# Optimization experiments

Hardware: AMD Instinct MI355X
Metric: run time of the kernel (lower is better)

## Reference

```python
import jax, jax.numpy as jnp
import numpy as np

B, N, C, H, WS, RANK = 64, 197, 768, 12, 14, 24
HD = C // H
SCALE = HD ** -0.5
NUM_REL = (2 * WS - 1) * (2 * WS - 1) + 3  # 732


def _make_rel_pos_index():
    coords = np.stack(np.meshgrid(np.arange(WS), np.arange(WS), indexing='ij'))  # [2,14,14]
    cf = coords.reshape(2, -1)  # [2,196]
    rel = (cf[:, :, None] - cf[:, None, :]).transpose(1, 2, 0)  # [196,196,2]
    rel = rel.copy()
    rel[..., 0] += WS - 1
    rel[..., 1] += WS - 1
    rel[..., 0] *= 2 * WS - 1
    idx = np.zeros((N, N), dtype=np.int32)
    idx[1:, 1:] = rel.sum(-1)
    idx[0, :] = NUM_REL - 3
    idx[:, 0] = NUM_REL - 2
    idx[0, 0] = NUM_REL - 1
    return idx


def setup_inputs() -> dict:
    key = jax.random.key(0)
    ks = jax.random.split(key, 13)
    s = lambda k, shape, sc=0.02: jax.random.normal(k, shape, jnp.float32) * sc
    return {
        'x': jax.random.normal(ks[0], (B, N, C), jnp.float32),
        'qkv_w': s(ks[1], (3 * C, C)),
        'q_bias': s(ks[2], (C,)),
        'v_bias': s(ks[3], (C,)),
        'q_lora_a': s(ks[4], (RANK, C)),
        'q_lora_b': s(ks[5], (C, RANK)),
        'k_lora_a': s(ks[6], (RANK, C)),
        'k_lora_b': s(ks[7], (C, RANK)),
        'v_lora_a': s(ks[8], (RANK, C)),
        'v_lora_b': s(ks[9], (C, RANK)),
        'rel_pos_table': s(ks[10], (NUM_REL, H)),
        'proj_w': s(ks[11], (C, C)),
        'proj_b': s(ks[12], (C,)),
        'rel_pos_index': jnp.asarray(_make_rel_pos_index()),
    }


def reference(x, qkv_w, q_bias, v_bias, q_lora_a, q_lora_b, k_lora_a, k_lora_b,
              v_lora_a, v_lora_b, rel_pos_table, proj_w, proj_b, rel_pos_index):
    lora = lambda a, b: jnp.einsum('bnc,rc,dr->bnd', x, a, b)  # rank-RANK adapter, scalar 1.0
    qkv_bias = jnp.concatenate([q_bias, jnp.zeros_like(v_bias), v_bias])
    qkv = x @ qkv_w.T + qkv_bias  # [B,N,3C]
    qkv = qkv + jnp.concatenate([lora(q_lora_a, q_lora_b),
                                 lora(k_lora_a, k_lora_b),
                                 lora(v_lora_a, v_lora_b)], axis=-1)
    qkv = qkv.reshape(B, N, 3, H, HD).transpose(2, 0, 3, 1, 4)  # [3,B,H,N,HD]
    q, k, v = qkv[0] * SCALE, qkv[1], qkv[2]
    attn = jnp.einsum('bhnd,bhmd->bhnm', q.astype(jnp.float32), k.astype(jnp.float32))
    rpb = rel_pos_table[rel_pos_index.reshape(-1)].reshape(N, N, H).transpose(2, 0, 1)
    attn = attn + rpb[None].astype(attn.dtype)
    attn = jax.nn.softmax(attn, axis=-1).astype(x.dtype)
    out = jnp.einsum('bhnm,bhmd->bhnd', attn, v).transpose(0, 2, 1, 3).reshape(B, N, C)
    return out @ proj_w.T + proj_b
```

## Files before the change

### kernel.cpp

```cpp
#include <hip/hip_runtime.h>

typedef __bf16 bf16;
typedef __attribute__((ext_vector_type(8))) __bf16 bf16x8;
typedef __attribute__((ext_vector_type(4))) __bf16 bf16x4;
typedef __attribute__((ext_vector_type(4))) float f32x4;

#define B_    64
#define N_    197
#define C_    768
#define H_    12
#define HD_   64
#define SCALE_ 0.125f
#define NM_   (N_*N_)
#define M_    (B_*N_)
#define NEGI_ (-30000.0f)
#define VTP_  200

#define GLL16(gptr, lptr) \
  __builtin_amdgcn_global_load_lds((const __attribute__((address_space(1))) unsigned int*)(gptr), \
                                   (__attribute__((address_space(3))) unsigned int*)(lptr), 16, 0, 0)

__global__ __launch_bounds__(256) void prep_kernel(
    const float* __restrict__ x, const float* __restrict__ pw,
    const float* __restrict__ qkv_w, const float* __restrict__ q_bias, const float* __restrict__ v_bias,
    const float* __restrict__ qa, const float* __restrict__ qb,
    const float* __restrict__ ka, const float* __restrict__ kb,
    const float* __restrict__ va, const float* __restrict__ vb,
    const float* __restrict__ table, const int* __restrict__ rpi,
    bf16* __restrict__ xbf, bf16* __restrict__ pwbf,
    bf16* __restrict__ weff, float* __restrict__ biasf, bf16* __restrict__ rpbT)
{
  const int bid = blockIdx.x, tid = threadIdx.x;
  if (bid < 5016) {
    const size_t n1 = (size_t)M_ * C_;
    size_t i8 = ((size_t)bid * 256 + tid) * 8;
    const float* src; bf16* dst; size_t off;
    if (i8 < n1) { src = x;  dst = xbf;  off = i8; }
    else         { src = pw; dst = pwbf; off = i8 - n1; }
    float4 f0 = *(const float4*)(src + off);
    float4 f1 = *(const float4*)(src + off + 4);
    bf16x8 v8;
    v8[0] = (bf16)f0.x; v8[1] = (bf16)f0.y; v8[2] = (bf16)f0.z; v8[3] = (bf16)f0.w;
    v8[4] = (bf16)f1.x; v8[5] = (bf16)f1.y; v8[6] = (bf16)f1.z; v8[7] = (bf16)f1.w;
    *(bf16x8*)(dst + off) = v8;
  } else if (bid < 11928) {
    int idx = (bid - 5016) * 256 + tid;
    int d = idx / C_, c = idx - d * C_;
    int sel = d / C_, dd = d - sel * C_;
    const float* a  = (sel == 0) ? qa : (sel == 1) ? ka : va;
    const float* bw = (sel == 0) ? qb : (sel == 1) ? kb : vb;
    float acc = qkv_w[idx];
#pragma unroll
    for (int r = 0; r < 24; ++r)
      acc += bw[dd * 24 + r] * a[r * C_ + c];
    weff[idx] = (bf16)acc;
    if (c == 0)
      biasf[d] = (sel == 0) ? q_bias[dd] : (sel == 2) ? v_bias[dd] : 0.0f;
  } else {
    int idx = (bid - 11928) * 256 + tid;
    if (idx < H_ * NM_) {
      int h = idx / NM_, nm = idx - h * NM_;
      int n = nm / N_, m = nm - n * N_;
      rpbT[((size_t)h * N_ + m) * VTP_ + n] = (bf16)table[rpi[nm] * H_ + h];
    }
  }
}

template<int MODE>
__global__ __launch_bounds__(256, 4) void gemm_bt(
    const bf16* __restrict__ A, const bf16* __restrict__ Bw,
    const float* __restrict__ biasp,
    float* __restrict__ Coutf, int M, int Nn, int K,
    bf16* __restrict__ qo, bf16* __restrict__ ko, bf16* __restrict__ vo)
{
  __shared__ __align__(16) bf16 As[128 * 64];
  __shared__ __align__(16) bf16 Bs[128 * 64];
  const int tid = threadIdx.x;
  const int lane = tid & 63, w = tid >> 6;
  const int l15 = lane & 15, quad = lane >> 4;
  const int wm = (w & 1) * 64, wn = (w >> 1) * 64;
  const int rowA0 = blockIdx.y * 128;
  const int rowB0 = blockIdx.x * 128;

  f32x4 acc[4][4] = {};

  for (int kt = 0; kt < K; kt += 64) {
#pragma unroll
    for (int i = 0; i < 4; ++i) {
      int lin = (w * 4 + i) * 64 + lane;
      int r  = lin >> 3;
      int cb = lin & 7;
      int csw = ((cb ^ (r & 7)) << 3);
      int ga = rowA0 + r; if (ga > M - 1) ga = M - 1;
      GLL16(A + (size_t)ga * K + kt + csw, &As[lin * 8]);
      int gb = rowB0 + r; if (gb > Nn - 1) gb = Nn - 1;
      GLL16(Bw + (size_t)gb * K + kt + csw, &Bs[lin * 8]);
    }
    __syncthreads();
#pragma unroll
    for (int ks = 0; ks < 2; ++ks) {
      const int cb = ks * 4 + quad;
      const int sw = (cb ^ (l15 & 7)) << 3;
      bf16x8 af[4], bfr[4];
#pragma unroll
      for (int i = 0; i < 4; ++i)
        af[i] = *(const bf16x8*)(&As[(wm + i * 16 + l15) * 64 + sw]);
#pragma unroll
      for (int j = 0; j < 4; ++j)
        bfr[j] = *(const bf16x8*)(&Bs[(wn + j * 16 + l15) * 64 + sw]);
#pragma unroll
      for (int i = 0; i < 4; ++i)
#pragma unroll
        for (int j = 0; j < 4; ++j)
          acc[i][j] = __builtin_amdgcn_mfma_f32_16x16x32_bf16(af[i], bfr[j], acc[i][j], 0, 0, 0);
    }
    __syncthreads();
  }

#pragma unroll
  for (int i = 0; i < 4; ++i) {
#pragma unroll
    for (int j = 0; j < 4; ++j) {
#pragma unroll
      for (int r = 0; r < 4; ++r) {
        int m = rowA0 + wm + i * 16 + quad * 4 + r;
        int d = rowB0 + wn + j * 16 + l15;
        if (m >= M) continue;
        float v = acc[i][j][r] + biasp[d];
        if (MODE == 0) {
          int b = m / N_, n = m - b * N_;
          int sel = d / C_, dd = d - sel * C_;
          int h = dd >> 6, hd = dd & 63;
          if (sel == 0)
            qo[(((size_t)b * H_ + h) * N_ + n) * HD_ + hd] = (bf16)(v * SCALE_);
          else if (sel == 1)
            ko[(((size_t)b * H_ + h) * N_ + n) * HD_ + hd] = (bf16)v;
          else
            vo[(((size_t)b * H_ + h) * HD_ + hd) * VTP_ + n] = (bf16)v;
        } else {
          Coutf[(size_t)m * Nn + d] = v;
        }
      }
    }
  }
}

#define SW 232
__global__ __launch_bounds__(256) void attn_kernel(
    const bf16* __restrict__ q, const bf16* __restrict__ k, const bf16* __restrict__ vT_g,
    const bf16* __restrict__ rpbT, bf16* __restrict__ out)
{
  __shared__ __align__(16) bf16 s_lds[64 * SW];

  const int tid = threadIdx.x;
  const int lane = tid & 63, w = tid >> 6;
  const int l15 = lane & 15, quad = lane >> 4;
  const int qt = blockIdx.x, h = blockIdx.y, b = blockIdx.z;
  const size_t bh = ((size_t)b * H_ + h) * N_ * HD_;
  const bf16* qb = q + bh;
  const bf16* kb = k + bh;
  const bf16* vg = vT_g + ((size_t)b * H_ + h) * HD_ * VTP_;

  if (quad < 2)
    *(uint4*)(&s_lds[(w * 16 + l15) * SW + 208 + quad * 8]) = (uint4){0, 0, 0, 0};

  const int row0 = qt * 64 + w * 16;
  int qm = row0 + l15; if (qm > N_ - 1) qm = N_ - 1;
  bf16x8 aq0 = *(const bf16x8*)(qb + qm * HD_ + quad * 8);
  bf16x8 aq1 = *(const bf16x8*)(qb + qm * HD_ + 32 + quad * 8);

  int rbase = row0 + quad * 4; if (rbase > N_ - 1) rbase = N_ - 1;

  float sum[4] = {0.f, 0.f, 0.f, 0.f};
#pragma unroll
  for (int jt = 0; jt < 13; ++jt) {
    int col = jt * 16 + l15;
    int kn = col; if (kn > N_ - 1) kn = N_ - 1;
    bf16x8 bk0 = *(const bf16x8*)(kb + kn * HD_ + quad * 8);
    bf16x8 bk1 = *(const bf16x8*)(kb + kn * HD_ + 32 + quad * 8);
    bf16x4 rb = *(const bf16x4*)(rpbT + ((size_t)h * N_ + kn) * VTP_ + rbase);
    f32x4 s = {0.f, 0.f, 0.f, 0.f};
    s = __builtin_amdgcn_mfma_f32_16x16x32_bf16(aq0, bk0, s, 0, 0, 0);
    s = __builtin_amdgcn_mfma_f32_16x16x32_bf16(aq1, bk1, s, 0, 0, 0);
#pragma unroll
    for (int r = 0; r < 4; ++r) {
      int row = row0 + quad * 4 + r;
      float sv = (col < N_ && row < N_) ? (s[r] + (float)rb[r]) : NEGI_;
      float p = __expf(sv);
      bf16 pb = (bf16)p;
      s_lds[(w * 16 + quad * 4 + r) * SW + col] = pb;
      sum[r] += (float)pb;
    }
  }

  bf16x8 bv0[4];
#pragma unroll
  for (int j2 = 0; j2 < 4; ++j2)
    bv0[j2] = *(const bf16x8*)(vg + (j2 * 16 + l15) * VTP_ + quad * 8);

#pragma unroll
  for (int r = 0; r < 4; ++r) {
    sum[r] += __shfl_xor(sum[r], 1);
    sum[r] += __shfl_xor(sum[r], 2);
    sum[r] += __shfl_xor(sum[r], 4);
    sum[r] += __shfl_xor(sum[r], 8);
  }
  float inv[4];
#pragma unroll
  for (int r = 0; r < 4; ++r) inv[r] = 1.0f / fmaxf(sum[r], 1e-20f);

  f32x4 o[4] = {};
  {
    bf16x8 ap = *(const bf16x8*)(&s_lds[(w * 16 + l15) * SW + quad * 8]);
#pragma unroll
    for (int j2 = 0; j2 < 4; ++j2)
      o[j2] = __builtin_amdgcn_mfma_f32_16x16x32_bf16(ap, bv0[j2], o[j2], 0, 0, 0);
  }
#pragma unroll
  for (int kk = 1; kk < 7; ++kk) {
    bf16x8 ap = *(const bf16x8*)(&s_lds[(w * 16 + l15) * SW + kk * 32 + quad * 8]);
#pragma unroll
    for (int j2 = 0; j2 < 4; ++j2) {
      bf16x8 bv = *(const bf16x8*)(vg + (j2 * 16 + l15) * VTP_ + kk * 32 + quad * 8);
      o[j2] = __builtin_amdgcn_mfma_f32_16x16x32_bf16(ap, bv, o[j2], 0, 0, 0);
    }
  }
#pragma unroll
  for (int j2 = 0; j2 < 4; ++j2) {
#pragma unroll
    for (int r = 0; r < 4; ++r) {
      int row = qt * 64 + w * 16 + quad * 4 + r;
      int hd = j2 * 16 + l15;
      if (row < N_)
        out[((size_t)b * N_ + row) * C_ + h * HD_ + hd] = (bf16)(o[j2][r] * inv[r]);
    }
  }
}

extern "C" void kernel_launch(void* const* d_in, const int* in_sizes, int n_in,
                              void* d_out, int out_size, void* d_ws, size_t ws_size,
                              hipStream_t stream)
{
  const float* x      = (const float*)d_in[0];
  const float* qkv_w  = (const float*)d_in[1];
  const float* q_bias = (const float*)d_in[2];
  const float* v_bias = (const float*)d_in[3];
  const float* q_la   = (const float*)d_in[4];
  const float* q_lb   = (const float*)d_in[5];
  const float* k_la   = (const float*)d_in[6];
  const float* k_lb   = (const float*)d_in[7];
  const float* v_la   = (const float*)d_in[8];
  const float* v_lb   = (const float*)d_in[9];
  const float* rpt    = (const float*)d_in[10];
  const float* proj_w = (const float*)d_in[11];
  const float* proj_b = (const float*)d_in[12];
  const int*   rpi    = (const int*)d_in[13];
  float* out = (float*)d_out;

  char* ws = (char*)d_ws;
  bf16*  xbf   = (bf16*)(ws);
  bf16*  aout  = (bf16*)(ws);
  bf16*  weff  = (bf16*)(ws + 19365888);
  float* biasf = (float*)(ws + 22904832);
  bf16*  pwbf  = (bf16*)(ws + 22914048);
  bf16*  qbuf  = (bf16*)(ws + 24093696);
  bf16*  kbuf  = (bf16*)(ws + 43459584);
  bf16*  vbufT = (bf16*)(ws + 62825472);
  bf16*  rpbT  = (bf16*)(ws + 82486400);

  prep_kernel<<<13748, 256, 0, stream>>>(
      x, proj_w, qkv_w, q_bias, v_bias, q_la, q_lb, k_la, k_lb, v_la, v_lb,
      rpt, rpi, xbf, pwbf, weff, biasf, rpbT);

  gemm_bt<0><<<dim3(18, 99), 256, 0, stream>>>(
      xbf, weff, biasf, nullptr, M_, 3 * C_, C_, qbuf, kbuf, vbufT);

  attn_kernel<<<dim3(4, H_, B_), 256, 0, stream>>>(qbuf, kbuf, vbufT, rpbT, aout);

  gemm_bt<1><<<dim3(6, 99), 256, 0, stream>>>(
      aout, pwbf, proj_b, out, M_, C_, C_, nullptr, nullptr, nullptr);
}
```

Baseline: 311.7 us.

## Add 256x256-tile pipelined QKV GEMM with XCD-aware block remap

Replaces the 128x128-tile QKV projection GEMM with a dedicated 512-thread kernel using 256x256 tiles. It double-buffers LDS with async global-to-LDS loads and splits each K-step into four quadrant phases so loads for the next tiles overlap MFMA work. It also remaps block IDs so neighbouring tiles land on the same XCD for L2 reuse. The large tile uses 128KB of LDS and many accumulator registers, and the grid shrinks to 450 blocks, which risks lower occupancy and wave-quantization loss in exchange for more data reuse per load.

```diff
diff --git a/kernel.cpp b/kernel.cpp
--- a/kernel.cpp
+++ b/kernel.cpp
@@ -66,6 +66,162 @@
   }
 }
 
+__global__ __launch_bounds__(512, 2) void gemm_qkv(
+    const bf16* __restrict__ A, const bf16* __restrict__ Bw,
+    const float* __restrict__ biasp, int M, int Nn, int K,
+    bf16* __restrict__ qo, bf16* __restrict__ ko, bf16* __restrict__ vo)
+{
+  __shared__ __align__(16) bf16 lds[2][2][256 * 64];
+  const int tid = threadIdx.x;
+  const int lane = tid & 63, w = tid >> 6;
+  const int l15 = lane & 15, quad = lane >> 4;
+  const int wm = w & 1;
+  const int wn = w >> 1;
+
+  const int nwg = gridDim.x, orig = blockIdx.x;
+  const int xcd = orig & 7, hi = orig >> 3;
+  const int qq = nwg >> 3, rr = nwg & 7;
+  const int wg = (xcd < rr ? xcd * (qq + 1) : rr * (qq + 1) + (xcd - rr) * qq) + hi;
+  const int ntx = Nn >> 8;
+  const int rowB0 = (wg % ntx) * 256;
+  const int rowA0 = (wg / ntx) * 256;
+
+  const int NT = K >> 6;
+  const int Mm = M - 1, Nm = Nn - 1;
+
+  f32x4 acc[8][4] = {};
+
+  auto stage = [&](const bf16* g, int grow0, int rmax, int kt, bf16* dst) {
+#pragma unroll
+    for (int i = 0; i < 2; ++i) {
+      int lin = i * 512 + tid;
+      int r = lin >> 3, cb = lin & 7;
+      int gr = grow0 + r; if (gr > rmax) gr = rmax;
+      GLL16(g + (size_t)gr * K + kt + ((cb ^ (r & 7)) << 3), dst + lin * 8);
+    }
+  };
+
+  stage(A,  rowA0,       Mm, 0, &lds[0][0][0]);
+  stage(A,  rowA0 + 128, Mm, 0, &lds[0][0][128 * 64]);
+  stage(Bw, rowB0,       Nm, 0, &lds[0][1][0]);
+  stage(Bw, rowB0 + 128, Nm, 0, &lds[0][1][128 * 64]);
+  if (NT > 1) {
+    stage(A, rowA0,       Mm, 64, &lds[1][0][0]);
+    stage(A, rowA0 + 128, Mm, 64, &lds[1][0][128 * 64]);
+  }
+  asm volatile("s_waitcnt vmcnt(4)" ::: "memory");
+  __builtin_amdgcn_s_barrier();
+
+  bf16x8 af[4][2], bl[2][2], bh[2][2];
+
+  for (int t = 0; t < NT; ++t) {
+    const int p = t & 1, q = p ^ 1;
+    const bf16* As = &lds[p][0][0];
+    const bf16* Bs = &lds[p][1][0];
+    auto rdA = [&](int mf, int kk) {
+      int row = wm * 128 + mf * 16 + l15;
+      int cb = kk * 4 + quad;
+      return *(const bf16x8*)(As + row * 64 + ((cb ^ (l15 & 7)) << 3));
+    };
+    auto rdB = [&](int nf, int kk) {
+      int row = wn * 64 + nf * 16 + l15;
+      int cb = kk * 4 + quad;
+      return *(const bf16x8*)(Bs + row * 64 + ((cb ^ (l15 & 7)) << 3));
+    };
+
+#pragma unroll
+    for (int mf = 0; mf < 4; ++mf) { af[mf][0] = rdA(mf, 0); af[mf][1] = rdA(mf, 1); }
+#pragma unroll
+    for (int nf = 0; nf < 2; ++nf) { bl[nf][0] = rdB(nf, 0); bl[nf][1] = rdB(nf, 1); }
+    if (t + 1 < NT) stage(Bw, rowB0, Nm, (t + 1) * 64, &lds[q][1][0]);
+    __builtin_amdgcn_s_barrier();
+    asm volatile("s_waitcnt lgkmcnt(0)" ::: "memory");
+    __builtin_amdgcn_s_setprio(1);
+#pragma unroll
+    for (int mf = 0; mf < 4; ++mf)
+#pragma unroll
+      for (int nf = 0; nf < 2; ++nf)
+#pragma unroll
+        for (int kk = 0; kk < 2; ++kk)
+          acc[mf][nf] = __builtin_amdgcn_mfma_f32_16x16x32_bf16(af[mf][kk], bl[nf][kk], acc[mf][nf], 0, 0, 0);
+    __builtin_amdgcn_s_setprio(0);
+    __builtin_amdgcn_s_barrier();
+
+#pragma unroll
+    for (int nf = 0; nf < 2; ++nf) { bh[nf][0] = rdB(nf + 2, 0); bh[nf][1] = rdB(nf + 2, 1); }
+    if (t + 1 < NT) stage(Bw, rowB0 + 128, Nm, (t + 1) * 64, &lds[q][1][128 * 64]);
+    __builtin_amdgcn_s_barrier();
+    asm volatile("s_waitcnt lgkmcnt(0)" ::: "memory");
+    __builtin_amdgcn_s_setprio(1);
+#pragma unroll
+    for (int mf = 0; mf < 4; ++mf)
+#pragma unroll
+      for (int nf = 0; nf < 2; ++nf)
+#pragma unroll
+        for (int kk = 0; kk < 2; ++kk)
+          acc[mf][nf + 2] = __builtin_amdgcn_mfma_f32_16x16x32_bf16(af[mf][kk], bh[nf][kk], acc[mf][nf + 2], 0, 0, 0);
+    __builtin_amdgcn_s_setprio(0);
+    __builtin_amdgcn_s_barrier();
+
+#pragma unroll
+    for (int mf = 0; mf < 4; ++mf) { af[mf][0] = rdA(mf + 4, 0); af[mf][1] = rdA(mf + 4, 1); }
+    if (t + 2 < NT) stage(A, rowA0, Mm, (t + 2) * 64, &lds[p][0][0]);
+    __builtin_amdgcn_s_barrier();
+    asm volatile("s_waitcnt lgkmcnt(0)" ::: "memory");
+    __builtin_amdgcn_s_setprio(1);
+#pragma unroll
+    for (int mf = 0; mf < 4; ++mf)
+#pragma unroll
+      for (int nf = 0; nf < 2; ++nf)
+#pragma unroll
+        for (int kk = 0; kk < 2; ++kk)
+          acc[mf + 4][nf + 2] = __builtin_amdgcn_mfma_f32_16x16x32_bf16(af[mf][kk], bh[nf][kk], acc[mf + 4][nf + 2], 0, 0, 0);
+    __builtin_amdgcn_s_setprio(0);
+    __builtin_amdgcn_s_barrier();
+
+#pragma unroll
+    for (int nf = 0; nf < 2; ++nf) { bl[nf][0] = rdB(nf, 0); bl[nf][1] = rdB(nf, 1); }
+    if (t + 2 < NT) stage(A, rowA0 + 128, Mm, (t + 2) * 64, &lds[p][0][128 * 64]);
+    __builtin_amdgcn_s_barrier();
+    asm volatile("s_waitcnt lgkmcnt(0)" ::: "memory");
+    __builtin_amdgcn_s_setprio(1);
+#pragma unroll
+    for (int mf = 0; mf < 4; ++mf)
+#pragma unroll
+      for (int nf = 0; nf < 2; ++nf)
+#pragma unroll
+        for (int kk = 0; kk < 2; ++kk)
+          acc[mf + 4][nf] = __builtin_amdgcn_mfma_f32_16x16x32_bf16(af[mf][kk], bl[nf][kk], acc[mf + 4][nf], 0, 0, 0);
+    __builtin_amdgcn_s_setprio(0);
+    if (t >= NT - 2) asm volatile("s_waitcnt vmcnt(0)" ::: "memory");
+    else             asm volatile("s_waitcnt vmcnt(4)" ::: "memory");
+    __builtin_amdgcn_s_barrier();
+  }
+
+#pragma unroll
+  for (int mf = 0; mf < 8; ++mf) {
+#pragma unroll
+    for (int nf = 0; nf < 4; ++nf) {
+#pragma unroll
+      for (int r = 0; r < 4; ++r) {
+        int m = rowA0 + wm * 128 + mf * 16 + quad * 4 + r;
+        int d = rowB0 + wn * 64 + nf * 16 + l15;
+        if (m >= M) continue;
+        float v = acc[mf][nf][r] + biasp[d];
+        int b = m / N_, n = m - b * N_;
+        int sel = d / C_, dd = d - sel * C_;
+        int h = dd >> 6, hd = dd & 63;
+        if (sel == 0)
+          qo[(((size_t)b * H_ + h) * N_ + n) * HD_ + hd] = (bf16)(v * SCALE_);
+        else if (sel == 1)
+          ko[(((size_t)b * H_ + h) * N_ + n) * HD_ + hd] = (bf16)v;
+        else
+          vo[(((size_t)b * H_ + h) * HD_ + hd) * VTP_ + n] = (bf16)v;
+      }
+    }
+  }
+}
+
 template<int MODE>
 __global__ __launch_bounds__(256, 4) void gemm_bt(
     const bf16* __restrict__ A, const bf16* __restrict__ Bw,
@@ -272,8 +428,8 @@
       x, proj_w, qkv_w, q_bias, v_bias, q_la, q_lb, k_la, k_lb, v_la, v_lb,
       rpt, rpi, xbf, pwbf, weff, biasf, rpbT);
 
-  gemm_bt<0><<<dim3(18, 99), 256, 0, stream>>>(
-      xbf, weff, biasf, nullptr, M_, 3 * C_, C_, qbuf, kbuf, vbufT);
+  gemm_qkv<<<dim3(450), 512, 0, stream>>>(
+      xbf, weff, biasf, M_, 3 * C_, C_, qbuf, kbuf, vbufT);
 
   attn_kernel<<<dim3(4, H_, B_), 256, 0, stream>>>(qbuf, kbuf, vbufT, rpbT, aout);
 
```

Result: slower. 348.8 us (+11.9%).

## Double-buffer LDS tiles in GEMM to overlap global loads with MFMA

Applied to the files above, without the earlier changes.

Gives the bf16 GEMM kernel two LDS buffers for the A and B tiles and prefetches the next K tile with global_load_lds while the MFMAs run on the current one. Each iteration now has a single barrier instead of two, and the load latency is meant to hide behind the compute. LDS use per block doubles to 64 KB, which may cut occupancy below the launch-bounds target of 4 blocks per CU.

```diff
diff --git a/kernel.cpp b/kernel.cpp
--- a/kernel.cpp
+++ b/kernel.cpp
@@ -73,30 +73,42 @@
     float* __restrict__ Coutf, int M, int Nn, int K,
     bf16* __restrict__ qo, bf16* __restrict__ ko, bf16* __restrict__ vo)
 {
-  __shared__ __align__(16) bf16 As[128 * 64];
-  __shared__ __align__(16) bf16 Bs[128 * 64];
+  __shared__ __align__(16) bf16 As[2][128 * 64];
+  __shared__ __align__(16) bf16 Bs[2][128 * 64];
   const int tid = threadIdx.x;
   const int lane = tid & 63, w = tid >> 6;
   const int l15 = lane & 15, quad = lane >> 4;
   const int wm = (w & 1) * 64, wn = (w >> 1) * 64;
   const int rowA0 = blockIdx.y * 128;
   const int rowB0 = blockIdx.x * 128;
+  const int NT = K >> 6;
+  const int Mm = M - 1, Nm = Nn - 1;
 
   f32x4 acc[4][4] = {};
 
-  for (int kt = 0; kt < K; kt += 64) {
+  auto stageAB = [&](int t, int p) {
+    const int kt = t * 64;
 #pragma unroll
     for (int i = 0; i < 4; ++i) {
       int lin = (w * 4 + i) * 64 + lane;
       int r  = lin >> 3;
       int cb = lin & 7;
       int csw = ((cb ^ (r & 7)) << 3);
-      int ga = rowA0 + r; if (ga > M - 1) ga = M - 1;
-      GLL16(A + (size_t)ga * K + kt + csw, &As[lin * 8]);
-      int gb = rowB0 + r; if (gb > Nn - 1) gb = Nn - 1;
-      GLL16(Bw + (size_t)gb * K + kt + csw, &Bs[lin * 8]);
-    }
-    __syncthreads();
+      int ga = rowA0 + r; if (ga > Mm) ga = Mm;
+      GLL16(A + (size_t)ga * K + kt + csw, &As[p][lin * 8]);
+      int gb = rowB0 + r; if (gb > Nm) gb = Nm;
+      GLL16(Bw + (size_t)gb * K + kt + csw, &Bs[p][lin * 8]);
+    }
+  };
+
+  stageAB(0, 0);
+  asm volatile("s_waitcnt vmcnt(0)" ::: "memory");
+  __builtin_amdgcn_s_barrier();
+  __builtin_amdgcn_sched_barrier(0);
+
+  for (int t = 0; t < NT; ++t) {
+    const int p = t & 1;
+    if (t + 1 < NT) stageAB(t + 1, p ^ 1);
 #pragma unroll
     for (int ks = 0; ks < 2; ++ks) {
       const int cb = ks * 4 + quad;
@@ -104,17 +116,19 @@
       bf16x8 af[4], bfr[4];
 #pragma unroll
       for (int i = 0; i < 4; ++i)
-        af[i] = *(const bf16x8*)(&As[(wm + i * 16 + l15) * 64 + sw]);
+        af[i] = *(const bf16x8*)(&As[p][(wm + i * 16 + l15) * 64 + sw]);
 #pragma unroll
       for (int j = 0; j < 4; ++j)
-        bfr[j] = *(const bf16x8*)(&Bs[(wn + j * 16 + l15) * 64 + sw]);
+        bfr[j] = *(const bf16x8*)(&Bs[p][(wn + j * 16 + l15) * 64 + sw]);
 #pragma unroll
       for (int i = 0; i < 4; ++i)
 #pragma unroll
         for (int j = 0; j < 4; ++j)
           acc[i][j] = __builtin_amdgcn_mfma_f32_16x16x32_bf16(af[i], bfr[j], acc[i][j], 0, 0, 0);
     }
-    __syncthreads();
+    if (t + 1 < NT) asm volatile("s_waitcnt vmcnt(0)" ::: "memory");
+    __builtin_amdgcn_s_barrier();
+    __builtin_amdgcn_sched_barrier(0);
   }
 
 #pragma unroll
```

Result: slower. 356.5 us (+14.4%).

## Drop LDS staging in GEMM; load MFMA fragments from global and remap tiles per XCD

Applied to the files above, without the earlier changes.

The GEMM no longer stages A and B tiles through shared memory with global_load_lds and barriers. Each lane now reads its bf16x8 MFMA fragments straight from global memory, relying on L1/L2 to serve the data other waves reuse. Workgroup IDs are also remapped so consecutive tiles land on the same XCD, which should improve L2 locality. The cost is more global and cache traffic, since every wave re-reads operand rows and there is no shared-memory reuse across waves, and there is no explicit prefetch.

```diff
diff --git a/kernel.cpp b/kernel.cpp
--- a/kernel.cpp
+++ b/kernel.cpp
@@ -15,10 +15,6 @@
 #define M_    (B_*N_)
 #define NEGI_ (-30000.0f)
 #define VTP_  200
-
-#define GLL16(gptr, lptr) \
-  __builtin_amdgcn_global_load_lds((const __attribute__((address_space(1))) unsigned int*)(gptr), \
-                                   (__attribute__((address_space(3))) unsigned int*)(lptr), 16, 0, 0)
 
 __global__ __launch_bounds__(256) void prep_kernel(
     const float* __restrict__ x, const float* __restrict__ pw,
@@ -73,48 +69,46 @@
     float* __restrict__ Coutf, int M, int Nn, int K,
     bf16* __restrict__ qo, bf16* __restrict__ ko, bf16* __restrict__ vo)
 {
-  __shared__ __align__(16) bf16 As[128 * 64];
-  __shared__ __align__(16) bf16 Bs[128 * 64];
   const int tid = threadIdx.x;
   const int lane = tid & 63, w = tid >> 6;
   const int l15 = lane & 15, quad = lane >> 4;
   const int wm = (w & 1) * 64, wn = (w >> 1) * 64;
-  const int rowA0 = blockIdx.y * 128;
-  const int rowB0 = blockIdx.x * 128;
+
+  const int ntx = gridDim.x;
+  const int nwg = ntx * gridDim.y;
+  int lid = blockIdx.y * ntx + blockIdx.x;
+  int xcd = lid & 7, hi = lid >> 3;
+  int qq = nwg >> 3, rr = nwg & 7;
+  int wg = (xcd < rr ? xcd * (qq + 1) : rr * (qq + 1) + (xcd - rr) * qq) + hi;
+  const int rowB0 = (wg % ntx) * 128;
+  const int rowA0 = (wg / ntx) * 128;
+
+  const bf16* pa[4]; const bf16* pb[4];
+#pragma unroll
+  for (int i = 0; i < 4; ++i) {
+    int ra = rowA0 + wm + i * 16 + l15; if (ra > M - 1) ra = M - 1;
+    pa[i] = A + (size_t)ra * K + quad * 8;
+    int rb = rowB0 + wn + i * 16 + l15; if (rb > Nn - 1) rb = Nn - 1;
+    pb[i] = Bw + (size_t)rb * K + quad * 8;
+  }
 
   f32x4 acc[4][4] = {};
 
   for (int kt = 0; kt < K; kt += 64) {
 #pragma unroll
-    for (int i = 0; i < 4; ++i) {
-      int lin = (w * 4 + i) * 64 + lane;
-      int r  = lin >> 3;
-      int cb = lin & 7;
-      int csw = ((cb ^ (r & 7)) << 3);
-      int ga = rowA0 + r; if (ga > M - 1) ga = M - 1;
-      GLL16(A + (size_t)ga * K + kt + csw, &As[lin * 8]);
-      int gb = rowB0 + r; if (gb > Nn - 1) gb = Nn - 1;
-      GLL16(Bw + (size_t)gb * K + kt + csw, &Bs[lin * 8]);
-    }
-    __syncthreads();
-#pragma unroll
     for (int ks = 0; ks < 2; ++ks) {
-      const int cb = ks * 4 + quad;
-      const int sw = (cb ^ (l15 & 7)) << 3;
       bf16x8 af[4], bfr[4];
 #pragma unroll
-      for (int i = 0; i < 4; ++i)
-        af[i] = *(const bf16x8*)(&As[(wm + i * 16 + l15) * 64 + sw]);
-#pragma unroll
-      for (int j = 0; j < 4; ++j)
-        bfr[j] = *(const bf16x8*)(&Bs[(wn + j * 16 + l15) * 64 + sw]);
+      for (int i = 0; i < 4; ++i) {
+        af[i]  = *(const bf16x8*)(pa[i] + kt + ks * 32);
+        bfr[i] = *(const bf16x8*)(pb[i] + kt + ks * 32);
+      }
 #pragma unroll
       for (int i = 0; i < 4; ++i)
 #pragma unroll
         for (int j = 0; j < 4; ++j)
           acc[i][j] = __builtin_amdgcn_mfma_f32_16x16x32_bf16(af[i], bfr[j], acc[i][j], 0, 0, 0);
     }
-    __syncthreads();
   }
 
 #pragma unroll
```

After: 466.4 us. +49.6%, slower.
